# Kernel optimization log

Hardware: AMD Instinct MI355X
Metric: run time of the kernel (lower is better)

Reference implementation:

```python
import jax, jax.numpy as jnp
import numpy as np

B, D_IN, D_OUT, N_SUBNET, G = 16384, 512, 512, 8, 2


def setup_inputs() -> dict:
    key = jax.random.key(0)
    k_x, k_g, k_w = jax.random.split(key, 3)
    x = jax.random.normal(k_x, (B, D_IN), dtype=jnp.float32)
    groups = jax.random.randint(k_g, (B, G), 0, N_SUBNET, dtype=jnp.int32)
    # per-expert Dense params (the 'subnets')
    W = jax.random.normal(k_w, (N_SUBNET, D_IN, D_OUT), dtype=jnp.float32) * (1.0 / np.sqrt(D_IN))
    b = jnp.zeros((N_SUBNET, D_OUT), dtype=jnp.float32)
    return {"x": x, "groups": groups, "W": W, "b": b}


def reference(x, groups, W, b):
    """SubnetGate: one-hot gated dispatch to per-group subnets + combine.

    Faithful math: gates = one_hot(groups[:, group_col], n_subnet);
    out = sum_e gates[:, e] * subnet_e(x). Since gates are one-hot the
    combine selects exactly one expert output per row (gate weight 1.0).
    """
    group_col = 0
    n_subnet = W.shape[0]
    idx_group = groups[:, group_col]                     # [B]
    gates = jax.nn.one_hot(idx_group, n_subnet, dtype=x.dtype)  # [B, E]
    # run every expert on the full batch (dense reference for the
    # gather-compute-scatter kernel), then gate-combine
    expert_out = jnp.einsum("bi,eio->beo", x, W) + b[None, :, :]  # [B, E, O]
    out = jnp.einsum("be,beo->bo", gates, expert_out)             # [B, O]
    return out
```

## Files before the change

### kernel.cpp

```cpp
#include <hip/hip_runtime.h>
#include <hip/hip_bf16.h>


#define NROWS   16384
#define KDIM    512
#define NDIM    512
#define NEXP    8
#define BM      128
#define BN      128
#define BK      64
#define APAD    72
#define WS_NDESC_OFF   64
#define WS_DESC_OFF    128
#define WS_ROWLIST_OFF 4096
#define WS_WT_OFF      (4096 + NEXP * NROWS * 4)

typedef __bf16        bf16x8 __attribute__((ext_vector_type(8)));
typedef float         f32x4  __attribute__((ext_vector_type(4)));
typedef unsigned int  u32x4  __attribute__((ext_vector_type(4)));

__device__ __forceinline__ unsigned int f2bf_u(float f) {
    unsigned int u = __builtin_bit_cast(unsigned int, f);
    return (u + 0x7FFFu + ((u >> 16) & 1u)) >> 16;
}

__device__ __forceinline__ u32x4 pack8(f32x4 a, f32x4 b) {
    u32x4 p;
    p.x = f2bf_u(a.x) | (f2bf_u(a.y) << 16);
    p.y = f2bf_u(a.z) | (f2bf_u(a.w) << 16);
    p.z = f2bf_u(b.x) | (f2bf_u(b.y) << 16);
    p.w = f2bf_u(b.z) | (f2bf_u(b.w) << 16);
    return p;
}

__global__ void zero_kernel(int* __restrict__ gcnt) {
    if (threadIdx.x < NEXP) gcnt[threadIdx.x] = 0;
}

__global__ void prep_kernel(const float* __restrict__ W,
                            const int* __restrict__ groups,
                            int* __restrict__ gcnt,
                            int* __restrict__ rowlist,
                            unsigned short* __restrict__ Wt) {
    __shared__ unsigned short tl[64 * 66];
    __shared__ int lcnt[NEXP];
    __shared__ int lbase[NEXP];
    const int bid = blockIdx.x;
    const int tid = threadIdx.x;

    if (bid < 512) {
        const int e  = bid >> 6;
        const int ot = (bid >> 3) & 7;
        const int it = bid & 7;
        const float*    Wb  = W  + (size_t)e * (KDIM * NDIM);
        unsigned short* Wtb = Wt + (size_t)e * (KDIM * NDIM);
        #pragma unroll
        for (int itr = 0; itr < 16; ++itr) {
            int f = itr * 256 + tid;
            int r = f >> 6, c = f & 63;
            tl[r * 66 + c] =
                (unsigned short)f2bf_u(Wb[(size_t)(it * 64 + r) * NDIM + ot * 64 + c]);
        }
        __syncthreads();
        #pragma unroll
        for (int itr = 0; itr < 16; ++itr) {
            int f = itr * 256 + tid;
            int r2 = f >> 6, c2 = f & 63;
            Wtb[(size_t)(ot * 64 + r2) * KDIM + it * 64 + c2] = tl[c2 * 66 + r2];
        }
    } else {
        const int base = (bid - 512) * 256;
        if (tid < NEXP) lcnt[tid] = 0;
        __syncthreads();
        int r = base + tid;
        int e = groups[r * 2];
        int pos = atomicAdd(&lcnt[e], 1);
        __syncthreads();
        if (tid < NEXP) lbase[tid] = atomicAdd(&gcnt[tid], lcnt[tid]);
        __syncthreads();
        rowlist[e * NROWS + lbase[e] + pos] = r;
    }
}

__global__ void plan_kernel(const int* __restrict__ counts,
                            int* __restrict__ ndesc,
                            int* __restrict__ desc) {
    if (threadIdx.x == 0) {
        int M = 0;
        for (int e = 0; e < NEXP; ++e) {
            int nmt = (counts[e] + BM - 1) / BM;
            for (int mt = 0; mt < nmt; ++mt) desc[M++] = (e << 16) | mt;
        }
        ndesc[0] = M;
    }
}

__global__ __launch_bounds__(256, 3)
void gemm_kernel(const float* __restrict__ x,
                 const int* __restrict__ counts,
                 const int* __restrict__ rowlist,
                 const unsigned short* __restrict__ Wt,
                 const float* __restrict__ bias,
                 float* __restrict__ out,
                 const int* __restrict__ ndesc,
                 const int* __restrict__ desc) {
    __shared__ __align__(16) unsigned short Asm[2][BM * APAD];

    const int tid = threadIdx.x;
    const int w   = tid >> 6;
    const int ln  = tid & 63;
    const int q   = ln >> 4;
    const int l15 = ln & 15;
    const int wm  = (w >> 1) * 64;
    const int wn  = (w & 1) * 64;

    const int T = ndesc[0] * 4;
    for (int t = blockIdx.x; t < T; t += gridDim.x) {
        const int d  = t >> 2;
        const int nt = t & 3;
        const int de = desc[d];
        const int e  = de >> 16;
        const int mt = de & 0xffff;
        const int cnt = counts[e];
        const int rb  = mt * BM;
        int m_valid = cnt - rb;
        if (m_valid > BM) m_valid = BM;
        const int* rl = rowlist + e * NROWS + rb;

        const float* srcp[4];
        int lm[4], lg[4];
        #pragma unroll
        for (int i = 0; i < 4; ++i) {
            int f = i * 256 + tid;
            lm[i] = f >> 3;
            lg[i] = f & 7;
            srcp[i] = (lm[i] < m_valid) ? (x + (size_t)rl[lm[i]] * KDIM + lg[i] * 8)
                                        : nullptr;
        }

        const unsigned short* We = Wt + (size_t)e * (KDIM * NDIM);
        const unsigned short* brow[4];
        #pragma unroll
        for (int ni = 0; ni < 4; ++ni)
            brow[ni] = We + (size_t)(nt * BN + wn + ni * 16 + l15) * KDIM;

        f32x4 acc[4][4];
        #pragma unroll
        for (int mi = 0; mi < 4; ++mi)
            #pragma unroll
            for (int ni = 0; ni < 4; ++ni)
                acc[mi][ni] = (f32x4){0.f, 0.f, 0.f, 0.f};

        #pragma unroll
        for (int i = 0; i < 4; ++i) {
            u32x4 p = {0u, 0u, 0u, 0u};
            if (srcp[i]) {
                f32x4 a = *(const f32x4*)(srcp[i]);
                f32x4 b = *(const f32x4*)(srcp[i] + 4);
                p = pack8(a, b);
            }
            *(u32x4*)&Asm[0][lm[i] * APAD + lg[i] * 8] = p;
        }
        __syncthreads();

        #pragma unroll 1
        for (int kt = 0; kt < 8; ++kt) {
            const int cur = kt & 1;
            f32x4 ga[4], gb[4];
            if (kt < 7) {
                #pragma unroll
                for (int i = 0; i < 4; ++i) {
                    if (srcp[i]) {
                        const float* s = srcp[i] + (kt + 1) * BK;
                        ga[i] = *(const f32x4*)s;
                        gb[i] = *(const f32x4*)(s + 4);
                    }
                }
            }
            #pragma unroll
            for (int ks = 0; ks < 2; ++ks) {
                const int g = ks * 4 + q;
                bf16x8 af[4], bfr[4];
                #pragma unroll
                for (int mi = 0; mi < 4; ++mi)
                    af[mi] = *(const bf16x8*)&Asm[cur][(wm + mi * 16 + l15) * APAD + g * 8];
                #pragma unroll
                for (int ni = 0; ni < 4; ++ni)
                    bfr[ni] = *(const bf16x8*)(brow[ni] + kt * BK + g * 8);
                #pragma unroll
                for (int mi = 0; mi < 4; ++mi)
                    #pragma unroll
                    for (int ni = 0; ni < 4; ++ni)
                        acc[mi][ni] = __builtin_amdgcn_mfma_f32_16x16x32_bf16(
                            af[mi], bfr[ni], acc[mi][ni], 0, 0, 0);
            }
            if (kt < 7) {
                #pragma unroll
                for (int i = 0; i < 4; ++i) {
                    u32x4 p = {0u, 0u, 0u, 0u};
                    if (srcp[i]) p = pack8(ga[i], gb[i]);
                    *(u32x4*)&Asm[cur ^ 1][lm[i] * APAD + lg[i] * 8] = p;
                }
            }
            __syncthreads();
        }

        int growv[16];
        #pragma unroll
        for (int mi = 0; mi < 4; ++mi)
            #pragma unroll
            for (int r = 0; r < 4; ++r) {
                int rloc = wm + mi * 16 + q * 4 + r;
                growv[mi * 4 + r] = (rloc < m_valid) ? rl[rloc] : -1;
            }
        const int ncol0 = nt * BN + wn;
        #pragma unroll
        for (int ni = 0; ni < 4; ++ni) {
            int col = ncol0 + ni * 16 + l15;
            float bv = bias[e * NDIM + col];
            #pragma unroll
            for (int mi = 0; mi < 4; ++mi)
                #pragma unroll
                for (int r = 0; r < 4; ++r) {
                    int gr = growv[mi * 4 + r];
                    if (gr >= 0) out[(size_t)gr * NDIM + col] = acc[mi][ni][r] + bv;
                }
        }
    }
}

extern "C" void kernel_launch(void* const* d_in, const int* in_sizes, int n_in,
                              void* d_out, int out_size, void* d_ws, size_t ws_size,
                              hipStream_t stream) {
    const float* x      = (const float*)d_in[0];
    const int*   groups = (const int*)d_in[1];
    const float* W      = (const float*)d_in[2];
    const float* b      = (const float*)d_in[3];
    float*       out    = (float*)d_out;

    char* ws = (char*)d_ws;
    int*            counts  = (int*)ws;
    int*            ndesc   = (int*)(ws + WS_NDESC_OFF);
    int*            desc    = (int*)(ws + WS_DESC_OFF);
    int*            rowlist = (int*)(ws + WS_ROWLIST_OFF);
    unsigned short* Wt      = (unsigned short*)(ws + WS_WT_OFF);

    zero_kernel<<<1, 64, 0, stream>>>(counts);
    prep_kernel<<<576, 256, 0, stream>>>(W, groups, counts, rowlist, Wt);
    plan_kernel<<<1, 64, 0, stream>>>(counts, ndesc, desc);
    gemm_kernel<<<544, 256, 0, stream>>>(x, counts, rowlist, Wt, b, out, ndesc, desc);
}
```

Measured before the change: 143.2 us.

## Pre-stage gathered x and W into MFMA fragment layout, drop LDS in GEMM

Adds a staging kernel that converts W to bf16 directly in MFMA-fragment order and gathers the routed rows of x into bf16 fragment-ordered tiles of 64 rows. The GEMM then has each wave independently load its fragments straight from global memory, with register double buffering and no LDS or block barriers, over 64-row tiles and smaller per-wave tiles. This is meant to remove the LDS staging, sync costs and strided B loads, at the cost of an extra kernel launch and an extra global round-trip for the gathered x. MAX_DESC also caps the number of tiles, which could silently drop rows if the expert distribution is very skewed.

```diff
diff --git a/kernel.cpp b/kernel.cpp
--- a/kernel.cpp
+++ b/kernel.cpp
@@ -6,14 +6,13 @@
 #define KDIM    512
 #define NDIM    512
 #define NEXP    8
-#define BM      128
-#define BN      128
-#define BK      64
-#define APAD    72
+#define MAX_DESC 264
 #define WS_NDESC_OFF   64
 #define WS_DESC_OFF    128
 #define WS_ROWLIST_OFF 4096
 #define WS_WT_OFF      (4096 + NEXP * NROWS * 4)
+#define WS_XG_OFF      (WS_WT_OFF + NEXP * KDIM * NDIM * 2)
+#define WS_NEED        ((size_t)WS_XG_OFF + (size_t)MAX_DESC * 8 * 4096 * 2)
 
 typedef __bf16        bf16x8 __attribute__((ext_vector_type(8)));
 typedef float         f32x4  __attribute__((ext_vector_type(4)));
@@ -23,13 +22,13 @@
     unsigned int u = __builtin_bit_cast(unsigned int, f);
     return (u + 0x7FFFu + ((u >> 16) & 1u)) >> 16;
 }
-
+__device__ __forceinline__ unsigned int pack2(float a, float b) {
+    return f2bf_u(a) | (f2bf_u(b) << 16);
+}
 __device__ __forceinline__ u32x4 pack8(f32x4 a, f32x4 b) {
     u32x4 p;
-    p.x = f2bf_u(a.x) | (f2bf_u(a.y) << 16);
-    p.y = f2bf_u(a.z) | (f2bf_u(a.w) << 16);
-    p.z = f2bf_u(b.x) | (f2bf_u(b.y) << 16);
-    p.w = f2bf_u(b.z) | (f2bf_u(b.w) << 16);
+    p.x = pack2(a.x, a.y); p.y = pack2(a.z, a.w);
+    p.z = pack2(b.x, b.y); p.w = pack2(b.z, b.w);
     return p;
 }
 
@@ -37,49 +36,22 @@
     if (threadIdx.x < NEXP) gcnt[threadIdx.x] = 0;
 }
 
-__global__ void prep_kernel(const float* __restrict__ W,
-                            const int* __restrict__ groups,
+__global__ void hist_kernel(const int* __restrict__ groups,
                             int* __restrict__ gcnt,
-                            int* __restrict__ rowlist,
-                            unsigned short* __restrict__ Wt) {
-    __shared__ unsigned short tl[64 * 66];
+                            int* __restrict__ rowlist) {
     __shared__ int lcnt[NEXP];
     __shared__ int lbase[NEXP];
-    const int bid = blockIdx.x;
     const int tid = threadIdx.x;
-
-    if (bid < 512) {
-        const int e  = bid >> 6;
-        const int ot = (bid >> 3) & 7;
-        const int it = bid & 7;
-        const float*    Wb  = W  + (size_t)e * (KDIM * NDIM);
-        unsigned short* Wtb = Wt + (size_t)e * (KDIM * NDIM);
-        #pragma unroll
-        for (int itr = 0; itr < 16; ++itr) {
-            int f = itr * 256 + tid;
-            int r = f >> 6, c = f & 63;
-            tl[r * 66 + c] =
-                (unsigned short)f2bf_u(Wb[(size_t)(it * 64 + r) * NDIM + ot * 64 + c]);
-        }
-        __syncthreads();
-        #pragma unroll
-        for (int itr = 0; itr < 16; ++itr) {
-            int f = itr * 256 + tid;
-            int r2 = f >> 6, c2 = f & 63;
-            Wtb[(size_t)(ot * 64 + r2) * KDIM + it * 64 + c2] = tl[c2 * 66 + r2];
-        }
-    } else {
-        const int base = (bid - 512) * 256;
-        if (tid < NEXP) lcnt[tid] = 0;
-        __syncthreads();
-        int r = base + tid;
-        int e = groups[r * 2];
-        int pos = atomicAdd(&lcnt[e], 1);
-        __syncthreads();
-        if (tid < NEXP) lbase[tid] = atomicAdd(&gcnt[tid], lcnt[tid]);
-        __syncthreads();
-        rowlist[e * NROWS + lbase[e] + pos] = r;
-    }
+    const int base = blockIdx.x * 256;
+    if (tid < NEXP) lcnt[tid] = 0;
+    __syncthreads();
+    int r = base + tid;
+    int e = groups[r * 2];
+    int pos = atomicAdd(&lcnt[e], 1);
+    __syncthreads();
+    if (tid < NEXP) lbase[tid] = atomicAdd(&gcnt[tid], lcnt[tid]);
+    __syncthreads();
+    rowlist[e * NROWS + lbase[e] + pos] = r;
 }
 
 __global__ void plan_kernel(const int* __restrict__ counts,
@@ -88,142 +60,165 @@
     if (threadIdx.x == 0) {
         int M = 0;
         for (int e = 0; e < NEXP; ++e) {
-            int nmt = (counts[e] + BM - 1) / BM;
-            for (int mt = 0; mt < nmt; ++mt) desc[M++] = (e << 16) | mt;
+            int nmt = (counts[e] + 63) >> 6;
+            for (int mt = 0; mt < nmt && M < MAX_DESC; ++mt)
+                desc[M++] = (e << 16) | mt;
         }
         ndesc[0] = M;
     }
 }
 
+__global__ __launch_bounds__(256, 4)
+void stage_kernel(const float* __restrict__ x,
+                  const float* __restrict__ W,
+                  const int* __restrict__ counts,
+                  const int* __restrict__ rowlist,
+                  const int* __restrict__ ndesc,
+                  const int* __restrict__ desc,
+                  unsigned short* __restrict__ Wf,
+                  unsigned short* __restrict__ xf) {
+    const int bid = blockIdx.x;
+    const int tid = threadIdx.x;
+
+    if (bid < 64) {
+        const int e  = bid >> 3;
+        const int kt = bid & 7;
+        const float* Wb = W + (size_t)e * (KDIM * NDIM);
+        unsigned short* dst = Wf + ((size_t)(e * 8 + kt)) * 32768;
+        #pragma unroll
+        for (int it = 0; it < 16; ++it) {
+            int gidx = it * 256 + tid;
+            int lane = gidx & 63;
+            int nf   = (gidx >> 6) & 31;
+            int kf   = gidx >> 11;
+            int q    = lane >> 4;
+            int l15  = lane & 15;
+            int n    = nf * 16 + l15;
+            int k0   = kt * 64 + kf * 32 + q * 8;
+            unsigned int p[4];
+            #pragma unroll
+            for (int jj = 0; jj < 4; ++jj)
+                p[jj] = pack2(Wb[(size_t)(k0 + 2 * jj) * NDIM + n],
+                              Wb[(size_t)(k0 + 2 * jj + 1) * NDIM + n]);
+            *(u32x4*)&dst[(size_t)gidx * 8] = *(const u32x4*)p;
+        }
+    } else {
+        const int b2 = bid - 64;
+        const int d  = b2 >> 3;
+        const int kt = b2 & 7;
+        if (d >= ndesc[0]) return;
+        const int de = desc[d];
+        const int e  = de >> 16;
+        const int mt = de & 0xffff;
+        int m_valid = counts[e] - mt * 64;
+        if (m_valid > 64) m_valid = 64;
+        const int* rl = rowlist + e * NROWS + mt * 64;
+        unsigned short* dst = xf + ((size_t)(d * 8 + kt)) * 4096;
+        #pragma unroll
+        for (int it = 0; it < 2; ++it) {
+            int gidx = it * 256 + tid;
+            int lane = gidx & 63;
+            int mf   = (gidx >> 6) & 3;
+            int kf   = gidx >> 8;
+            int q    = lane >> 4;
+            int l15  = lane & 15;
+            int m    = mf * 16 + l15;
+            u32x4 p = {0u, 0u, 0u, 0u};
+            if (m < m_valid) {
+                const float* s = x + (size_t)rl[m] * KDIM + kt * 64 + kf * 32 + q * 8;
+                p = pack8(*(const f32x4*)s, *(const f32x4*)(s + 4));
+            }
+            *(u32x4*)&dst[(size_t)gidx * 8] = p;
+        }
+    }
+}
+
 __global__ __launch_bounds__(256, 3)
-void gemm_kernel(const float* __restrict__ x,
-                 const int* __restrict__ counts,
-                 const int* __restrict__ rowlist,
-                 const unsigned short* __restrict__ Wt,
-                 const float* __restrict__ bias,
-                 float* __restrict__ out,
-                 const int* __restrict__ ndesc,
-                 const int* __restrict__ desc) {
-    __shared__ __align__(16) unsigned short Asm[2][BM * APAD];
-
+void gemm_frag(const unsigned short* __restrict__ xf,
+               const int* __restrict__ counts,
+               const int* __restrict__ rowlist,
+               const unsigned short* __restrict__ Wf,
+               const float* __restrict__ bias,
+               float* __restrict__ out,
+               const int* __restrict__ ndesc,
+               const int* __restrict__ desc) {
     const int tid = threadIdx.x;
     const int w   = tid >> 6;
     const int ln  = tid & 63;
     const int q   = ln >> 4;
     const int l15 = ln & 15;
-    const int wm  = (w >> 1) * 64;
-    const int wn  = (w & 1) * 64;
-
-    const int T = ndesc[0] * 4;
-    for (int t = blockIdx.x; t < T; t += gridDim.x) {
-        const int d  = t >> 2;
-        const int nt = t & 3;
+
+    const int Twaves = ndesc[0] * 16;
+    for (int wt = blockIdx.x * 4 + w; wt < Twaves; wt += gridDim.x * 4) {
+        const int d     = wt >> 4;
+        const int half  = (wt >> 3) & 1;
+        const int strip = wt & 7;
         const int de = desc[d];
         const int e  = de >> 16;
         const int mt = de & 0xffff;
-        const int cnt = counts[e];
-        const int rb  = mt * BM;
-        int m_valid = cnt - rb;
-        if (m_valid > BM) m_valid = BM;
-        const int* rl = rowlist + e * NROWS + rb;
-
-        const float* srcp[4];
-        int lm[4], lg[4];
-        #pragma unroll
-        for (int i = 0; i < 4; ++i) {
-            int f = i * 256 + tid;
-            lm[i] = f >> 3;
-            lg[i] = f & 7;
-            srcp[i] = (lm[i] < m_valid) ? (x + (size_t)rl[lm[i]] * KDIM + lg[i] * 8)
-                                        : nullptr;
-        }
-
-        const unsigned short* We = Wt + (size_t)e * (KDIM * NDIM);
-        const unsigned short* brow[4];
-        #pragma unroll
-        for (int ni = 0; ni < 4; ++ni)
-            brow[ni] = We + (size_t)(nt * BN + wn + ni * 16 + l15) * KDIM;
-
-        f32x4 acc[4][4];
-        #pragma unroll
-        for (int mi = 0; mi < 4; ++mi)
+        int m_valid = counts[e] - mt * 64;
+        if (m_valid > 64) m_valid = 64;
+        const int* rl = rowlist + e * NROWS + mt * 64;
+
+        const unsigned short* ab = xf + (size_t)d * 32768 + (half * 2) * 512 + ln * 8;
+        const unsigned short* bb = Wf + (size_t)e * 262144 + (strip * 4) * 512 + ln * 8;
+
+        f32x4 acc[2][4];
+        #pragma unroll
+        for (int mi = 0; mi < 2; ++mi)
             #pragma unroll
             for (int ni = 0; ni < 4; ++ni)
                 acc[mi][ni] = (f32x4){0.f, 0.f, 0.f, 0.f};
 
-        #pragma unroll
-        for (int i = 0; i < 4; ++i) {
-            u32x4 p = {0u, 0u, 0u, 0u};
-            if (srcp[i]) {
-                f32x4 a = *(const f32x4*)(srcp[i]);
-                f32x4 b = *(const f32x4*)(srcp[i] + 4);
-                p = pack8(a, b);
+        bf16x8 af[2][2], bv[2][4];
+        #pragma unroll
+        for (int mi = 0; mi < 2; ++mi)
+            af[0][mi] = *(const bf16x8*)(ab + mi * 512);
+        #pragma unroll
+        for (int ni = 0; ni < 4; ++ni)
+            bv[0][ni] = *(const bf16x8*)(bb + ni * 512);
+
+        #pragma unroll
+        for (int s = 0; s < 16; ++s) {
+            const int buf = s & 1;
+            if (s < 15) {
+                const int s1 = s + 1;
+                const int kt = s1 >> 1, kf = s1 & 1;
+                const unsigned short* a1 = ab + kt * 4096 + kf * 2048;
+                const unsigned short* b1 = bb + kt * 32768 + kf * 16384;
+                #pragma unroll
+                for (int mi = 0; mi < 2; ++mi)
+                    af[buf ^ 1][mi] = *(const bf16x8*)(a1 + mi * 512);
+                #pragma unroll
+                for (int ni = 0; ni < 4; ++ni)
+                    bv[buf ^ 1][ni] = *(const bf16x8*)(b1 + ni * 512);
             }
-            *(u32x4*)&Asm[0][lm[i] * APAD + lg[i] * 8] = p;
-        }
-        __syncthreads();
-
-        #pragma unroll 1
-        for (int kt = 0; kt < 8; ++kt) {
-            const int cur = kt & 1;
-            f32x4 ga[4], gb[4];
-            if (kt < 7) {
-                #pragma unroll
-                for (int i = 0; i < 4; ++i) {
-                    if (srcp[i]) {
-                        const float* s = srcp[i] + (kt + 1) * BK;
-                        ga[i] = *(const f32x4*)s;
-                        gb[i] = *(const f32x4*)(s + 4);
-                    }
-                }
-            }
-            #pragma unroll
-            for (int ks = 0; ks < 2; ++ks) {
-                const int g = ks * 4 + q;
-                bf16x8 af[4], bfr[4];
-                #pragma unroll
-                for (int mi = 0; mi < 4; ++mi)
-                    af[mi] = *(const bf16x8*)&Asm[cur][(wm + mi * 16 + l15) * APAD + g * 8];
+            #pragma unroll
+            for (int mi = 0; mi < 2; ++mi)
                 #pragma unroll
                 for (int ni = 0; ni < 4; ++ni)
-                    bfr[ni] = *(const bf16x8*)(brow[ni] + kt * BK + g * 8);
-                #pragma unroll
-                for (int mi = 0; mi < 4; ++mi)
-                    #pragma unroll
-                    for (int ni = 0; ni < 4; ++ni)
-                        acc[mi][ni] = __builtin_amdgcn_mfma_f32_16x16x32_bf16(
-                            af[mi], bfr[ni], acc[mi][ni], 0, 0, 0);
-            }
-            if (kt < 7) {
-                #pragma unroll
-                for (int i = 0; i < 4; ++i) {
-                    u32x4 p = {0u, 0u, 0u, 0u};
-                    if (srcp[i]) p = pack8(ga[i], gb[i]);
-                    *(u32x4*)&Asm[cur ^ 1][lm[i] * APAD + lg[i] * 8] = p;
-                }
-            }
-            __syncthreads();
-        }
-
-        int growv[16];
-        #pragma unroll
-        for (int mi = 0; mi < 4; ++mi)
+                    acc[mi][ni] = __builtin_amdgcn_mfma_f32_16x16x32_bf16(
+                        af[buf][mi], bv[buf][ni], acc[mi][ni], 0, 0, 0);
+        }
+
+        int growv[8];
+        #pragma unroll
+        for (int mi = 0; mi < 2; ++mi)
             #pragma unroll
             for (int r = 0; r < 4; ++r) {
-                int rloc = wm + mi * 16 + q * 4 + r;
+                int rloc = half * 32 + mi * 16 + q * 4 + r;
                 growv[mi * 4 + r] = (rloc < m_valid) ? rl[rloc] : -1;
             }
-        const int ncol0 = nt * BN + wn;
         #pragma unroll
         for (int ni = 0; ni < 4; ++ni) {
-            int col = ncol0 + ni * 16 + l15;
-            float bv = bias[e * NDIM + col];
-            #pragma unroll
-            for (int mi = 0; mi < 4; ++mi)
+            int col = strip * 64 + ni * 16 + l15;
+            float bvs = bias[e * NDIM + col];
+            #pragma unroll
+            for (int mi = 0; mi < 2; ++mi)
                 #pragma unroll
                 for (int r = 0; r < 4; ++r) {
                     int gr = growv[mi * 4 + r];
-                    if (gr >= 0) out[(size_t)gr * NDIM + col] = acc[mi][ni][r] + bv;
+                    if (gr >= 0) out[(size_t)gr * NDIM + col] = acc[mi][ni][r] + bvs;
                 }
         }
     }
@@ -243,10 +238,14 @@
     int*            ndesc   = (int*)(ws + WS_NDESC_OFF);
     int*            desc    = (int*)(ws + WS_DESC_OFF);
     int*            rowlist = (int*)(ws + WS_ROWLIST_OFF);
-    unsigned short* Wt      = (unsigned short*)(ws + WS_WT_OFF);
+    unsigned short* Wf      = (unsigned short*)(ws + WS_WT_OFF);
+    unsigned short* xf      = (unsigned short*)(ws + WS_XG_OFF);
 
     zero_kernel<<<1, 64, 0, stream>>>(counts);
-    prep_kernel<<<576, 256, 0, stream>>>(W, groups, counts, rowlist, Wt);
+    hist_kernel<<<64, 256, 0, stream>>>(groups, counts, rowlist);
     plan_kernel<<<1, 64, 0, stream>>>(counts, ndesc, desc);
-    gemm_kernel<<<544, 256, 0, stream>>>(x, counts, rowlist, Wt, b, out, ndesc, desc);
-}
+    stage_kernel<<<64 + MAX_DESC * 8, 256, 0, stream>>>(x, W, counts, rowlist,
+                                                        ndesc, desc, Wf, xf);
+    gemm_frag<<<1056, 256, 0, stream>>>(xf, counts, rowlist, Wf, b, out,
+                                        ndesc, desc);
+}
```

Result: faster. 132.6 us (-7.4%).
